# Performance work log

Hardware: AMD Instinct MI355X
Metric: run time of the kernel (lower is better)

The kernel has to match this reference:

```python
import jax, jax.numpy as jnp
import numpy as np

N = 100000   # nodes
E = 1600000  # edges
D = 128      # in_dim
H = 128      # hidden_dim
C = 40       # num_classes
EPS = 1e-5   # LayerNorm eps (torch default)


def setup_inputs() -> dict:
    key = jax.random.key(0)
    ks = jax.random.split(key, 16)
    x = jax.random.normal(ks[0], (N, D), dtype=jnp.float32)
    edge_index = jax.random.randint(ks[1], (2, E), 0, N, dtype=jnp.int64)
    s = 1.0 / np.sqrt(D)
    inp = {"x": x, "edge_index": edge_index}
    # 3 GCN layers: weight [in, H], bias [H]; LayerNorm gamma/beta [H]
    for i in range(3):
        inp[f"W{i}"] = jax.random.normal(ks[2 + i], (D if i == 0 else H, H), dtype=jnp.float32) * s
        inp[f"b{i}"] = jnp.zeros((H,), jnp.float32)
        inp[f"g{i}"] = jnp.ones((H,), jnp.float32)
        inp[f"be{i}"] = jnp.zeros((H,), jnp.float32)
    inp["Wc"] = jax.random.normal(ks[10], (H, C), dtype=jnp.float32) * (1.0 / np.sqrt(H))
    inp["bc"] = jnp.zeros((C,), jnp.float32)
    return inp


def _layer_norm(h, g, b):
    mu = jnp.mean(h, axis=-1, keepdims=True)
    var = jnp.var(h, axis=-1, keepdims=True)  # biased, matches torch
    return (h - mu) * jax.lax.rsqrt(var + EPS) * g + b


def _gcn_conv(x, W, b, src, dst, enorm, dinv2):
    # GCNConv: D^{-1/2}(A+I)D^{-1/2} X W + b (self-loops handled analytically)
    h = x @ W                                   # [N, H]
    agg = jax.ops.segment_sum(h[src] * enorm[:, None], dst, num_segments=N)
    return agg + h * dinv2[:, None] + b


def reference(x, edge_index, W0, b0, g0, be0, W1, b1, g1, be1, W2, b2, g2, be2, Wc, bc):
    src, dst = edge_index[0], edge_index[1]
    # degree with self-loops (GCNConv adds self-loops by default)
    deg = jnp.zeros((N,), x.dtype).at[dst].add(1.0) + 1.0
    dinv = jax.lax.rsqrt(deg)
    enorm = dinv[src] * dinv[dst]               # per-edge normalization
    dinv2 = dinv * dinv                         # self-loop normalization

    Ws, bs, gs, bes = (W0, W1, W2), (b0, b1, b2), (g0, g1, g2), (be0, be1, be2)
    for i in range(3):
        x_in = x
        x = _gcn_conv(x, Ws[i], bs[i], src, dst, enorm, dinv2)
        x = _layer_norm(x, gs[i], bes[i])
        x = jax.nn.elu(x)
        if i > 0:
            x = x + x_in
        # dropout: eval mode / p=0 -> identity
    return x @ Wc + bc
```

## Files before the change

kernel.cpp:

```cpp
#include <hip/hip_runtime.h>
#include <math.h>

#define N_NODES 100000
#define N_EDGES 1600000
#define DIM     128
#define NCLS    40
#define NBUCK   391
#define P1_CH   4096
#define CAP     8192

typedef _Float16 f16x8 __attribute__((ext_vector_type(8)));
typedef _Float16 f16x2 __attribute__((ext_vector_type(2)));
typedef float    f32x4 __attribute__((ext_vector_type(4)));

__device__ inline unsigned short f16bits(float f) {
    union { _Float16 h; unsigned short u; } cv;
    cv.h = (_Float16)f;
    return cv.u;
}
__device__ inline f16x2 as_h2(unsigned u) {
    union { unsigned u; f16x2 h; } cv;
    cv.u = u;
    return cv.h;
}
__device__ inline unsigned as_u(f16x2 h) {
    union { f16x2 h; unsigned u; } cv;
    cv.h = h;
    return cv.u;
}
__device__ inline unsigned pack_h2(float lo, float hi) {
    f16x2 h;
    h.x = (_Float16)lo;
    h.y = (_Float16)hi;
    return as_u(h);
}
__device__ inline int wave_incl_scan(int v, int lane) {
#pragma unroll
    for (int off = 1; off < 64; off <<= 1) {
        int x = __shfl_up(v, off, 64);
        if (lane >= off) v += x;
    }
    return v;
}

__global__ __launch_bounds__(256) void setup_p1(const float* __restrict__ W0,
                                                const float* __restrict__ W1,
                                                const float* __restrict__ W2,
                                                const float* __restrict__ Wc,
                                                const int* __restrict__ ei,
                                                unsigned short* __restrict__ Wsw0,
                                                unsigned short* __restrict__ Wsw1,
                                                unsigned short* __restrict__ Wsw2,
                                                unsigned short* __restrict__ Wcsw,
                                                int* __restrict__ bcnt,
                                                unsigned* __restrict__ tmp,
                                                unsigned short* __restrict__ H2) {
    const int blk = blockIdx.x;
    const int t   = threadIdx.x;

    if (blk < 192) {
        const float* W = (blk < 64) ? W0 : (blk < 128) ? W1 : W2;
        unsigned short* Wsw = (blk < 64) ? Wsw0 : (blk < 128) ? Wsw1 : Wsw2;
        int o = (blk & 63) * 256 + t;
        int f = o >> 9;
        int l = (o >> 3) & 63;
        int j = o & 7;
        int n = f >> 2;
        int s = f & 3;
        int k = s * 32 + (l >> 4) * 8 + j;
        int c = (l & 15) * 8 + n;
        Wsw[o] = f16bits(W[k * DIM + c]);
        return;
    }
    if (blk < 216) {
        int o = (blk - 192) * 256 + t;
        int f = o >> 9;
        int l = (o >> 3) & 63;
        int j = o & 7;
        int n = f >> 2;
        int s = f & 3;
        int k = s * 32 + (l >> 4) * 8 + j;
        int c = (l & 15) * 3 + n;
        Wcsw[o] = (c < NCLS) ? f16bits(Wc[k * NCLS + c]) : (unsigned short)0;
        return;
    }
    if (blk == 216) {
        uint4* p = (uint4*)(H2 + (size_t)N_NODES * DIM);
        uint4 zz = make_uint4(0u, 0u, 0u, 0u);
#pragma unroll
        for (int i = 0; i < 4; ++i) p[t + i * 256] = zz;
        return;
    }

    __shared__ int  hist[512];
    __shared__ int  lscan[512];
    __shared__ int  rank_[512];
    __shared__ int  gbase[512];
    __shared__ int  wtA[4];
    __shared__ int2 stage[P1_CH];

    const int lane = t & 63, wv = t >> 6;
    const int e0  = (blk - 217) * P1_CH;
    const int cnt = min(P1_CH, N_EDGES - e0);

    hist[t] = 0;
    hist[t + 256] = 0;
    __syncthreads();

    int2 ed[16];
#pragma unroll
    for (int i = 0; i < 16; ++i) {
        int idx = t + i * 256;
        if (idx < cnt) {
            ed[i] = make_int2(ei[e0 + idx], ei[N_EDGES + e0 + idx]);
            atomicAdd(&hist[ed[i].y >> 8], 1);
        }
    }
    __syncthreads();

    int h0 = hist[2 * t], h1 = hist[2 * t + 1];
    int pvA = h0 + h1;
    int iA = wave_incl_scan(pvA, lane);
    if (lane == 63) wtA[wv] = iA;
    __syncthreads();
    {
        int fA = 0;
        for (int i = 0; i < wv; ++i) fA += wtA[i];
        iA += fA;
    }
    int eA = iA - pvA;
    lscan[2 * t]     = eA;
    lscan[2 * t + 1] = eA + h0;
    rank_[2 * t]     = eA;
    rank_[2 * t + 1] = eA + h0;
    if (h0) {
        int off = atomicAdd(&bcnt[2 * t], h0);
        if (off > CAP - h0) off = CAP - h0;
        if (off < 0) off = 0;
        gbase[2 * t] = (2 * t) * CAP + off;
    }
    if (h1) {
        int off = atomicAdd(&bcnt[2 * t + 1], h1);
        if (off > CAP - h1) off = CAP - h1;
        if (off < 0) off = 0;
        gbase[2 * t + 1] = (2 * t + 1) * CAP + off;
    }
    __syncthreads();

#pragma unroll
    for (int i = 0; i < 16; ++i) {
        int idx = t + i * 256;
        if (idx < cnt) {
            int b = ed[i].y >> 8;
            int p = atomicAdd(&rank_[b], 1);
            stage[p] = ed[i];
        }
    }
    __syncthreads();

    for (int p = t; p < cnt; p += 256) {
        int2 v = stage[p];
        int b = v.y >> 8;
        int dstidx = gbase[b] + (p - lscan[b]);
        if (dstidx < (b + 1) * CAP)
            tmp[dstidx] = ((unsigned)v.x << 8) | ((unsigned)v.y & 255u);
    }
}

__global__ __launch_bounds__(256) void csr_p2_gemm(const unsigned* __restrict__ tmp,
                                                   const int* __restrict__ bcnt,
                                                   const float* __restrict__ X,
                                                   const unsigned short* __restrict__ Wsw,
                                                   int* __restrict__ rowptr,
                                                   float* __restrict__ dinv,
                                                   unsigned* __restrict__ rec,
                                                   unsigned short* __restrict__ H) {
    __shared__ unsigned short wlds[32 * 512];
    __shared__ int   cnt2[256];
    __shared__ int   cur[256];
    __shared__ float dv_s[256];
    __shared__ int   wt[4];
    __shared__ int   sbeg_s;
    const int t = threadIdx.x;
    const int lane = t & 63, wv = t >> 6;
    const int b = blockIdx.x;

    {
        const uint4* srcp = (const uint4*)Wsw;
        uint4*       dstp = (uint4*)wlds;
#pragma unroll
        for (int i = 0; i < 8; ++i) dstp[t + i * 256] = srcp[t + i * 256];
    }

    int v0 = min(bcnt[2 * t], CAP), v1 = min(bcnt[2 * t + 1], CAP);
    int pv = v0 + v1;
    int incl = wave_incl_scan(pv, lane);
    if (lane == 63) wt[wv] = incl;
    cnt2[t] = 0;
    __syncthreads();
    {
        int pf = 0;
        for (int i = 0; i < wv; ++i) pf += wt[i];
        incl += pf;
        int eB = incl - pv;
        if (2 * t == b)     sbeg_s = eB;
        if (2 * t + 1 == b) sbeg_s = eB + v0;
    }
    __syncthreads();

    const int m = min(bcnt[b], CAP);
    const unsigned* tb = tmp + (size_t)b * CAP;
    for (int idx = t; idx < m; idx += 256)
        atomicAdd(&cnt2[tb[idx] & 255u], 1);
    __syncthreads();

    int c = cnt2[t];
    int incl2 = wave_incl_scan(c, lane);
    if (lane == 63) wt[wv] = incl2;
    __syncthreads();
    {
        int pf = 0;
        for (int i = 0; i < wv; ++i) pf += wt[i];
        incl2 += pf;
    }
    int rb = sbeg_s + (incl2 - c);
    cur[t] = rb;
    float dv = rsqrtf((float)c + 1.0f);
    dv_s[t] = dv;
    const int node = (b << 8) + t;
    if (node < N_NODES) {
        rowptr[node] = rb;
        dinv[node]   = dv;
    }
    if (b == NBUCK - 1 && t == 0) rowptr[N_NODES] = N_EDGES;
    __syncthreads();

    for (int idx = t; idx < m; idx += 256) {
        unsigned u = tb[idx];
        int pos = atomicAdd(&cur[u & 255u], 1);
        if ((unsigned)pos < (unsigned)N_EDGES)
            rec[pos] = (u >> 8) << 8;
    }

    const int mq = lane & 15;
    const int q  = lane >> 4;
    const int rowbase = (b << 8) + wv * 64;

    for (int r4 = 0; r4 < 4; ++r4) {
        const int row0 = rowbase + r4 * 16;
        int r = row0 + mq;
        if (r >= N_NODES) r = N_NODES - 1;
        const float* xp = X + (size_t)r * DIM + q * 8;
        f16x8 af[4];
#pragma unroll
        for (int s = 0; s < 4; ++s) {
            float4 x0 = *(const float4*)(xp + s * 32);
            float4 x1 = *(const float4*)(xp + s * 32 + 4);
            f16x8 v;
            v[0] = (_Float16)x0.x; v[1] = (_Float16)x0.y;
            v[2] = (_Float16)x0.z; v[3] = (_Float16)x0.w;
            v[4] = (_Float16)x1.x; v[5] = (_Float16)x1.y;
            v[6] = (_Float16)x1.z; v[7] = (_Float16)x1.w;
            af[s] = v;
        }

        f32x4 acc[8];
        f32x4 z = {0.f, 0.f, 0.f, 0.f};
#pragma unroll
        for (int n = 0; n < 8; ++n) acc[n] = z;

        const unsigned short* wl = wlds + lane * 8;
#pragma unroll
        for (int s = 0; s < 4; ++s)
#pragma unroll
            for (int n = 0; n < 8; ++n) {
                f16x8 wf = *(const f16x8*)(wl + ((n * 4 + s) << 9));
                acc[n] = __builtin_amdgcn_mfma_f32_16x16x32_f16(af[s], wf, acc[n], 0, 0, 0);
            }

#pragma unroll
        for (int j = 0; j < 4; ++j) {
            int row = row0 + q * 4 + j;
            if (row < N_NODES) {
                float dvr = dv_s[row - (b << 8)];
                uint4 o;
                o.x = pack_h2(acc[0][j] * dvr, acc[1][j] * dvr);
                o.y = pack_h2(acc[2][j] * dvr, acc[3][j] * dvr);
                o.z = pack_h2(acc[4][j] * dvr, acc[5][j] * dvr);
                o.w = pack_h2(acc[6][j] * dvr, acc[7][j] * dvr);
                *(uint4*)(H + (size_t)row * DIM + mq * 8) = o;
            } else if (row < N_NODES + 32) {
                uint4 zz = make_uint4(0u, 0u, 0u, 0u);
                *(uint4*)(H + (size_t)row * DIM + mq * 8) = zz;
            }
        }
    }
}

__global__ __launch_bounds__(256) void agg_ln_gemm(const unsigned short* __restrict__ Hh,
                                                   const unsigned short* __restrict__ xin,
                                                   const float* __restrict__ dinv,
                                                   const float* __restrict__ bias,
                                                   const float* __restrict__ g,
                                                   const float* __restrict__ be,
                                                   const int* __restrict__ rowptr,
                                                   const unsigned* __restrict__ rec,
                                                   const unsigned short* __restrict__ Wsw,
                                                   unsigned short* __restrict__ Cout,
                                                   unsigned short* __restrict__ Hout) {
    __shared__ _Float16 hl[16][136];
    const int tid  = threadIdx.x;
    const int lane = tid & 63;
    const int l16  = tid & 15;
    const int gb   = lane & 48;
    const int grp  = tid >> 4;
    const int wave = tid >> 6;
    const int node0 = blockIdx.x * 16;
    const int node = node0 + grp;
    const int beg  = rowptr[node];
    const int end  = rowptr[node + 1];
    const char* Hb8 = (const char*)Hh;
    const unsigned laneoff = (unsigned)l16 * 16;
    const unsigned sentin  = (unsigned)N_NODES << 8;

    f16x2 accA[4], accB[4], accC[4], accD[4];
    f16x2 hz = {(_Float16)0.f, (_Float16)0.f};
#pragma unroll
    for (int k = 0; k < 4; ++k) { accA[k] = hz; accB[k] = hz; accC[k] = hz; accD[k] = hz; }

    for (int e0 = beg; e0 < end; e0 += 16) {
        int cnt = min(end - e0, 16);
        unsigned sv = (l16 < cnt) ? rec[e0 + l16] : sentin;
        int cntR = (cnt + 7) & ~7;
        for (int j = 0; j < cntR; j += 8) {
            unsigned o0 = (unsigned)__shfl((int)sv, gb + j + 0, 64) + laneoff;
            unsigned o1 = (unsigned)__shfl((int)sv, gb + j + 1, 64) + laneoff;
            unsigned o2 = (unsigned)__shfl((int)sv, gb + j + 2, 64) + laneoff;
            unsigned o3 = (unsigned)__shfl((int)sv, gb + j + 3, 64) + laneoff;
            unsigned o4 = (unsigned)__shfl((int)sv, gb + j + 4, 64) + laneoff;
            unsigned o5 = (unsigned)__shfl((int)sv, gb + j + 5, 64) + laneoff;
            unsigned o6 = (unsigned)__shfl((int)sv, gb + j + 6, 64) + laneoff;
            unsigned o7 = (unsigned)__shfl((int)sv, gb + j + 7, 64) + laneoff;
            uint4 u0 = *(const uint4*)(Hb8 + o0);
            uint4 u1 = *(const uint4*)(Hb8 + o1);
            uint4 u2 = *(const uint4*)(Hb8 + o2);
            uint4 u3 = *(const uint4*)(Hb8 + o3);
            uint4 u4 = *(const uint4*)(Hb8 + o4);
            uint4 u5 = *(const uint4*)(Hb8 + o5);
            uint4 u6 = *(const uint4*)(Hb8 + o6);
            uint4 u7 = *(const uint4*)(Hb8 + o7);
            accA[0] += as_h2(u0.x); accA[1] += as_h2(u0.y); accA[2] += as_h2(u0.z); accA[3] += as_h2(u0.w);
            accB[0] += as_h2(u1.x); accB[1] += as_h2(u1.y); accB[2] += as_h2(u1.z); accB[3] += as_h2(u1.w);
            accC[0] += as_h2(u2.x); accC[1] += as_h2(u2.y); accC[2] += as_h2(u2.z); accC[3] += as_h2(u2.w);
            accD[0] += as_h2(u3.x); accD[1] += as_h2(u3.y); accD[2] += as_h2(u3.z); accD[3] += as_h2(u3.w);
            accA[0] += as_h2(u4.x); accA[1] += as_h2(u4.y); accA[2] += as_h2(u4.z); accA[3] += as_h2(u4.w);
            accB[0] += as_h2(u5.x); accB[1] += as_h2(u5.y); accB[2] += as_h2(u5.z); accB[3] += as_h2(u5.w);
            accC[0] += as_h2(u6.x); accC[1] += as_h2(u6.y); accC[2] += as_h2(u6.z); accC[3] += as_h2(u6.w);
            accD[0] += as_h2(u7.x); accD[1] += as_h2(u7.y); accD[2] += as_h2(u7.z); accD[3] += as_h2(u7.w);
        }
    }

#pragma unroll
    for (int k = 0; k < 4; ++k) accA[k] = (accA[k] + accB[k]) + (accC[k] + accD[k]);

    const float dv = dinv[node];
    const unsigned nodeoff = ((unsigned)node << 8) + laneoff;
    uint4 hv = *(const uint4*)(Hb8 + nodeoff);
    const int c0 = l16 * 8;
    float4 bb0 = *(const float4*)(bias + c0);
    float4 bb1 = *(const float4*)(bias + c0 + 4);
    f16x2 h0 = as_h2(hv.x), h1 = as_h2(hv.y), h2 = as_h2(hv.z), h3 = as_h2(hv.w);

    float a[8];
    a[0] = ((float)accA[0].x + (float)h0.x) * dv + bb0.x;
    a[1] = ((float)accA[0].y + (float)h0.y) * dv + bb0.y;
    a[2] = ((float)accA[1].x + (float)h1.x) * dv + bb0.z;
    a[3] = ((float)accA[1].y + (float)h1.y) * dv + bb0.w;
    a[4] = ((float)accA[2].x + (float)h2.x) * dv + bb1.x;
    a[5] = ((float)accA[2].y + (float)h2.y) * dv + bb1.y;
    a[6] = ((float)accA[3].x + (float)h3.x) * dv + bb1.z;
    a[7] = ((float)accA[3].y + (float)h3.y) * dv + bb1.w;

    float s1 = 0.f, s2 = 0.f;
#pragma unroll
    for (int i = 0; i < 8; ++i) { s1 += a[i]; s2 += a[i] * a[i]; }
#pragma unroll
    for (int mk = 1; mk <= 8; mk <<= 1) {
        s1 += __shfl_xor(s1, mk, 64);
        s2 += __shfl_xor(s2, mk, 64);
    }
    float mean = s1 * (1.0f / 128.0f);
    float var  = s2 * (1.0f / 128.0f) - mean * mean;
    float rr   = rsqrtf(var + 1e-5f);

    float4 gg0 = *(const float4*)(g + c0);
    float4 gg1 = *(const float4*)(g + c0 + 4);
    float4 ee0 = *(const float4*)(be + c0);
    float4 ee1 = *(const float4*)(be + c0 + 4);

    float r[8];
    r[0] = (a[0] - mean) * rr * gg0.x + ee0.x;
    r[1] = (a[1] - mean) * rr * gg0.y + ee0.y;
    r[2] = (a[2] - mean) * rr * gg0.z + ee0.z;
    r[3] = (a[3] - mean) * rr * gg0.w + ee0.w;
    r[4] = (a[4] - mean) * rr * gg1.x + ee1.x;
    r[5] = (a[5] - mean) * rr * gg1.y + ee1.y;
    r[6] = (a[6] - mean) * rr * gg1.z + ee1.z;
    r[7] = (a[7] - mean) * rr * gg1.w + ee1.w;
#pragma unroll
    for (int i = 0; i < 8; ++i) r[i] = r[i] > 0.0f ? r[i] : expm1f(r[i]);

    if (xin) {
        uint4 xv = *(const uint4*)((const char*)xin + nodeoff);
        f16x2 x0 = as_h2(xv.x), x1 = as_h2(xv.y), x2 = as_h2(xv.z), x3 = as_h2(xv.w);
        r[0] += (float)x0.x; r[1] += (float)x0.y;
        r[2] += (float)x1.x; r[3] += (float)x1.y;
        r[4] += (float)x2.x; r[5] += (float)x2.y;
        r[6] += (float)x3.x; r[7] += (float)x3.y;
    }

    uint4 o;
    o.x = pack_h2(r[0], r[1]);
    o.y = pack_h2(r[2], r[3]);
    o.z = pack_h2(r[4], r[5]);
    o.w = pack_h2(r[6], r[7]);
    *(uint4*)((char*)Cout + nodeoff) = o;
    *(uint4*)&hl[grp][l16 * 8] = o;
    __syncthreads();

    {
        const int m = lane & 15;
        const int q = lane >> 4;

        f16x8 af[4];
#pragma unroll
        for (int s = 0; s < 4; ++s)
            af[s] = *(const f16x8*)&hl[m][q * 8 + s * 32];

        f32x4 acc2[2];
        f32x4 z = {0.f, 0.f, 0.f, 0.f};
        acc2[0] = z; acc2[1] = z;

#pragma unroll
        for (int s = 0; s < 4; ++s)
#pragma unroll
            for (int p = 0; p < 2; ++p) {
                f16x8 wfv = *(const f16x8*)(Wsw + (((2 * wave + p) * 4 + s) << 9) + lane * 8);
                acc2[p] = __builtin_amdgcn_mfma_f32_16x16x32_f16(af[s], wfv, acc2[p], 0, 0, 0);
            }

#pragma unroll
        for (int j = 0; j < 4; ++j) {
            int row = node0 + q * 4 + j;
            float dv2 = dinv[row];
            *(unsigned*)((char*)Hout + ((unsigned)row << 8) + ((unsigned)(m * 8 + 2 * wave) << 1)) =
                pack_h2(acc2[0][j] * dv2, acc2[1][j] * dv2);
        }
    }
}

__global__ __launch_bounds__(256) void agg_ln_cls(const unsigned short* __restrict__ Hh,
                                                  const unsigned short* __restrict__ xin,
                                                  const float* __restrict__ dinv,
                                                  const float* __restrict__ bias,
                                                  const float* __restrict__ g,
                                                  const float* __restrict__ be,
                                                  const int* __restrict__ rowptr,
                                                  const unsigned* __restrict__ rec,
                                                  const unsigned short* __restrict__ Wcsw,
                                                  const float* __restrict__ bc,
                                                  float* __restrict__ out) {
    __shared__ _Float16 hl[16][136];
    const int tid  = threadIdx.x;
    const int lane = tid & 63;
    const int l16  = tid & 15;
    const int gb   = lane & 48;
    const int grp  = tid >> 4;
    const int node0 = blockIdx.x * 16;
    const int node = node0 + grp;
    const int beg  = rowptr[node];
    const int end  = rowptr[node + 1];
    const char* Hb8 = (const char*)Hh;
    const unsigned laneoff = (unsigned)l16 * 16;
    const unsigned sentin  = (unsigned)N_NODES << 8;

    f16x2 accA[4], accB[4], accC[4], accD[4];
    f16x2 hz = {(_Float16)0.f, (_Float16)0.f};
#pragma unroll
    for (int k = 0; k < 4; ++k) { accA[k] = hz; accB[k] = hz; accC[k] = hz; accD[k] = hz; }

    for (int e0 = beg; e0 < end; e0 += 16) {
        int cnt = min(end - e0, 16);
        unsigned sv = (l16 < cnt) ? rec[e0 + l16] : sentin;
        int cntR = (cnt + 7) & ~7;
        for (int j = 0; j < cntR; j += 8) {
            unsigned o0 = (unsigned)__shfl((int)sv, gb + j + 0, 64) + laneoff;
            unsigned o1 = (unsigned)__shfl((int)sv, gb + j + 1, 64) + laneoff;
            unsigned o2 = (unsigned)__shfl((int)sv, gb + j + 2, 64) + laneoff;
            unsigned o3 = (unsigned)__shfl((int)sv, gb + j + 3, 64) + laneoff;
            unsigned o4 = (unsigned)__shfl((int)sv, gb + j + 4, 64) + laneoff;
            unsigned o5 = (unsigned)__shfl((int)sv, gb + j + 5, 64) + laneoff;
            unsigned o6 = (unsigned)__shfl((int)sv, gb + j + 6, 64) + laneoff;
            unsigned o7 = (unsigned)__shfl((int)sv, gb + j + 7, 64) + laneoff;
            uint4 u0 = *(const uint4*)(Hb8 + o0);
            uint4 u1 = *(const uint4*)(Hb8 + o1);
            uint4 u2 = *(const uint4*)(Hb8 + o2);
            uint4 u3 = *(const uint4*)(Hb8 + o3);
            uint4 u4 = *(const uint4*)(Hb8 + o4);
            uint4 u5 = *(const uint4*)(Hb8 + o5);
            uint4 u6 = *(const uint4*)(Hb8 + o6);
            uint4 u7 = *(const uint4*)(Hb8 + o7);
            accA[0] += as_h2(u0.x); accA[1] += as_h2(u0.y); accA[2] += as_h2(u0.z); accA[3] += as_h2(u0.w);
            accB[0] += as_h2(u1.x); accB[1] += as_h2(u1.y); accB[2] += as_h2(u1.z); accB[3] += as_h2(u1.w);
            accC[0] += as_h2(u2.x); accC[1] += as_h2(u2.y); accC[2] += as_h2(u2.z); accC[3] += as_h2(u2.w);
            accD[0] += as_h2(u3.x); accD[1] += as_h2(u3.y); accD[2] += as_h2(u3.z); accD[3] += as_h2(u3.w);
            accA[0] += as_h2(u4.x); accA[1] += as_h2(u4.y); accA[2] += as_h2(u4.z); accA[3] += as_h2(u4.w);
            accB[0] += as_h2(u5.x); accB[1] += as_h2(u5.y); accB[2] += as_h2(u5.z); accB[3] += as_h2(u5.w);
            accC[0] += as_h2(u6.x); accC[1] += as_h2(u6.y); accC[2] += as_h2(u6.z); accC[3] += as_h2(u6.w);
            accD[0] += as_h2(u7.x); accD[1] += as_h2(u7.y); accD[2] += as_h2(u7.z); accD[3] += as_h2(u7.w);
        }
    }

#pragma unroll
    for (int k = 0; k < 4; ++k) accA[k] = (accA[k] + accB[k]) + (accC[k] + accD[k]);

    const float dv = dinv[node];
    const unsigned nodeoff = ((unsigned)node << 8) + laneoff;
    uint4 hv = *(const uint4*)(Hb8 + nodeoff);
    const int c0 = l16 * 8;
    float4 bb0 = *(const float4*)(bias + c0);
    float4 bb1 = *(const float4*)(bias + c0 + 4);
    f16x2 h0 = as_h2(hv.x), h1 = as_h2(hv.y), h2 = as_h2(hv.z), h3 = as_h2(hv.w);

    float a[8];
    a[0] = ((float)accA[0].x + (float)h0.x) * dv + bb0.x;
    a[1] = ((float)accA[0].y + (float)h0.y) * dv + bb0.y;
    a[2] = ((float)accA[1].x + (float)h1.x) * dv + bb0.z;
    a[3] = ((float)accA[1].y + (float)h1.y) * dv + bb0.w;
    a[4] = ((float)accA[2].x + (float)h2.x) * dv + bb1.x;
    a[5] = ((float)accA[2].y + (float)h2.y) * dv + bb1.y;
    a[6] = ((float)accA[3].x + (float)h3.x) * dv + bb1.z;
    a[7] = ((float)accA[3].y + (float)h3.y) * dv + bb1.w;

    float s1 = 0.f, s2 = 0.f;
#pragma unroll
    for (int i = 0; i < 8; ++i) { s1 += a[i]; s2 += a[i] * a[i]; }
#pragma unroll
    for (int mk = 1; mk <= 8; mk <<= 1) {
        s1 += __shfl_xor(s1, mk, 64);
        s2 += __shfl_xor(s2, mk, 64);
    }
    float mean = s1 * (1.0f / 128.0f);
    float var  = s2 * (1.0f / 128.0f) - mean * mean;
    float rr   = rsqrtf(var + 1e-5f);

    float4 gg0 = *(const float4*)(g + c0);
    float4 gg1 = *(const float4*)(g + c0 + 4);
    float4 ee0 = *(const float4*)(be + c0);
    float4 ee1 = *(const float4*)(be + c0 + 4);

    float r[8];
    r[0] = (a[0] - mean) * rr * gg0.x + ee0.x;
    r[1] = (a[1] - mean) * rr * gg0.y + ee0.y;
    r[2] = (a[2] - mean) * rr * gg0.z + ee0.z;
    r[3] = (a[3] - mean) * rr * gg0.w + ee0.w;
    r[4] = (a[4] - mean) * rr * gg1.x + ee1.x;
    r[5] = (a[5] - mean) * rr * gg1.y + ee1.y;
    r[6] = (a[6] - mean) * rr * gg1.z + ee1.z;
    r[7] = (a[7] - mean) * rr * gg1.w + ee1.w;
#pragma unroll
    for (int i = 0; i < 8; ++i) r[i] = r[i] > 0.0f ? r[i] : expm1f(r[i]);

    if (xin) {
        uint4 xv = *(const uint4*)((const char*)xin + nodeoff);
        f16x2 x0 = as_h2(xv.x), x1 = as_h2(xv.y), x2 = as_h2(xv.z), x3 = as_h2(xv.w);
        r[0] += (float)x0.x; r[1] += (float)x0.y;
        r[2] += (float)x1.x; r[3] += (float)x1.y;
        r[4] += (float)x2.x; r[5] += (float)x2.y;
        r[6] += (float)x3.x; r[7] += (float)x3.y;
    }

    uint4 o;
    o.x = pack_h2(r[0], r[1]);
    o.y = pack_h2(r[2], r[3]);
    o.z = pack_h2(r[4], r[5]);
    o.w = pack_h2(r[6], r[7]);
    *(uint4*)&hl[grp][l16 * 8] = o;
    __syncthreads();

    if (tid < 64) {
        const int m = lane & 15;
        const int q = lane >> 4;

        f16x8 wf[12];
#pragma unroll
        for (int f = 0; f < 12; ++f)
            wf[f] = *(const f16x8*)(Wcsw + (f << 9) + lane * 8);

        f16x8 af[4];
#pragma unroll
        for (int s = 0; s < 4; ++s)
            af[s] = *(const f16x8*)&hl[m][q * 8 + s * 32];

        f32x4 acc[3];
        f32x4 z = {0.f, 0.f, 0.f, 0.f};
#pragma unroll
        for (int n = 0; n < 3; ++n) acc[n] = z;

#pragma unroll
        for (int s = 0; s < 4; ++s)
#pragma unroll
            for (int n = 0; n < 3; ++n)
                acc[n] = __builtin_amdgcn_mfma_f32_16x16x32_f16(af[s], wf[n * 4 + s], acc[n], 0, 0, 0);

#pragma unroll
        for (int j = 0; j < 4; ++j) {
            int row = node0 + q * 4 + j;
#pragma unroll
            for (int n = 0; n < 3; ++n) {
                int c = 3 * m + n;
                if (c < NCLS)
                    out[(size_t)row * NCLS + c] = acc[n][j] + bc[c];
            }
        }
    }
}

extern "C" void kernel_launch(void* const* d_in, const int* in_sizes, int n_in,
                              void* d_out, int out_size, void* d_ws, size_t ws_size,
                              hipStream_t stream) {
    const float* x  = (const float*)d_in[0];
    const int*   ei = (const int*)d_in[1];
    const float* W[3]  = {(const float*)d_in[2], (const float*)d_in[6], (const float*)d_in[10]};
    const float* b[3]  = {(const float*)d_in[3], (const float*)d_in[7], (const float*)d_in[11]};
    const float* g[3]  = {(const float*)d_in[4], (const float*)d_in[8], (const float*)d_in[12]};
    const float* be[3] = {(const float*)d_in[5], (const float*)d_in[9], (const float*)d_in[13]};
    const float* Wc = (const float*)d_in[14];
    const float* bc = (const float*)d_in[15];
    float* out = (float*)d_out;

    char* ws = (char*)d_ws;
    const size_t NP = 400128;
    float* dinv   = (float*)(ws);
    int*   rowptr = (int*)  (ws + NP);
    int*   bcnt   = (int*)  (ws + 2 * NP);
    unsigned* rec = (unsigned*)(ws + 2 * NP + 4096);
    unsigned short* H1 = (unsigned short*)(ws + 2 * NP + 4096 + (size_t)N_EDGES * 8);
    unsigned short* H2 = H1 + (size_t)(N_NODES + 64) * DIM;
    unsigned short* Ch = H2 + (size_t)(N_NODES + 64) * DIM;
    unsigned short* Wsw0 = Ch + (size_t)N_NODES * DIM;
    unsigned short* Wsw1 = Wsw0 + DIM * DIM;
    unsigned short* Wsw2 = Wsw1 + DIM * DIM;
    unsigned short* Wcsw = Wsw2 + DIM * DIM;
    unsigned* tmp = (unsigned*)Ch;

    hipMemsetAsync(bcnt, 0, 2048, stream);

    setup_p1<<<217 + NBUCK, 256, 0, stream>>>(W[0], W[1], W[2], Wc, ei,
                                              Wsw0, Wsw1, Wsw2, Wcsw, bcnt, tmp, H2);

    csr_p2_gemm<<<NBUCK, 256, 0, stream>>>(tmp, bcnt, x, Wsw0, rowptr, dinv, rec, H1);

    const int agg_grid = N_NODES / 16;

    agg_ln_gemm<<<agg_grid, 256, 0, stream>>>(H1, nullptr, dinv, b[0], g[0], be[0],
                                              rowptr, rec, Wsw1, Ch, H2);

    agg_ln_gemm<<<agg_grid, 256, 0, stream>>>(H2, Ch, dinv, b[1], g[1], be[1],
                                              rowptr, rec, Wsw2, Ch, H1);

    agg_ln_cls<<<agg_grid, 256, 0, stream>>>(H1, Ch, dinv, b[2], g[2], be[2],
                                             rowptr, rec, Wcsw, bc, out);
}
```

Before: 365.7 us.

## Replace global atomic bucket offsets with per-chunk count matrix and fixed slots

Edge binning no longer reserves space in each destination bucket with global atomics. Each edge chunk writes its per-bucket histogram into a bucket-by-chunk count matrix and places its edges in a fixed 32-entry slot per (bucket, chunk). A new small reduction kernel sums the matrix rows into bucket totals, and the CSR pass walks the padded slots, skipping empty entries. This removes the memset and the global atomics and makes the layout deterministic. In exchange it adds a kernel launch, more padded reads in the CSR pass, and silently drops edges if any chunk puts more than 32 edges into one bucket.

```diff
diff --git a/kernel.cpp b/kernel.cpp
--- a/kernel.cpp
+++ b/kernel.cpp
@@ -7,7 +7,7 @@
 #define NCLS    40
 #define NBUCK   391
 #define P1_CH   4096
-#define CAP     8192
+#define CAPB    32
 
 typedef _Float16 f16x8 __attribute__((ext_vector_type(8)));
 typedef _Float16 f16x2 __attribute__((ext_vector_type(2)));
@@ -52,7 +52,7 @@
                                                 unsigned short* __restrict__ Wsw1,
                                                 unsigned short* __restrict__ Wsw2,
                                                 unsigned short* __restrict__ Wcsw,
-                                                int* __restrict__ bcnt,
+                                                int* __restrict__ cntmat,
                                                 unsigned* __restrict__ tmp,
                                                 unsigned short* __restrict__ H2) {
     const int blk = blockIdx.x;
@@ -95,12 +95,12 @@
     __shared__ int  hist[512];
     __shared__ int  lscan[512];
     __shared__ int  rank_[512];
-    __shared__ int  gbase[512];
     __shared__ int  wtA[4];
     __shared__ int2 stage[P1_CH];
 
     const int lane = t & 63, wv = t >> 6;
-    const int e0  = (blk - 217) * P1_CH;
+    const int k   = blk - 217;
+    const int e0  = k * P1_CH;
     const int cnt = min(P1_CH, N_EDGES - e0);
 
     hist[t] = 0;
@@ -133,18 +133,8 @@
     lscan[2 * t + 1] = eA + h0;
     rank_[2 * t]     = eA;
     rank_[2 * t + 1] = eA + h0;
-    if (h0) {
-        int off = atomicAdd(&bcnt[2 * t], h0);
-        if (off > CAP - h0) off = CAP - h0;
-        if (off < 0) off = 0;
-        gbase[2 * t] = (2 * t) * CAP + off;
-    }
-    if (h1) {
-        int off = atomicAdd(&bcnt[2 * t + 1], h1);
-        if (off > CAP - h1) off = CAP - h1;
-        if (off < 0) off = 0;
-        gbase[2 * t + 1] = (2 * t + 1) * CAP + off;
-    }
+    if (2 * t < NBUCK)     cntmat[(size_t)(2 * t) * NBUCK + k]     = h0;
+    if (2 * t + 1 < NBUCK) cntmat[(size_t)(2 * t + 1) * NBUCK + k] = h1;
     __syncthreads();
 
 #pragma unroll
@@ -161,13 +151,28 @@
     for (int p = t; p < cnt; p += 256) {
         int2 v = stage[p];
         int b = v.y >> 8;
-        int dstidx = gbase[b] + (p - lscan[b]);
-        if (dstidx < (b + 1) * CAP)
-            tmp[dstidx] = ((unsigned)v.x << 8) | ((unsigned)v.y & 255u);
-    }
+        int r = p - lscan[b];
+        if (r < CAPB)
+            tmp[((size_t)b * NBUCK + k) * CAPB + r] = ((unsigned)v.x << 8) | ((unsigned)v.y & 255u);
+    }
+}
+
+__global__ __launch_bounds__(256) void bsum(const int* __restrict__ cntmat,
+                                            int* __restrict__ bcnt) {
+    const int gw   = (blockIdx.x * 256 + threadIdx.x) >> 6;
+    const int lane = threadIdx.x & 63;
+    int s = 0;
+    if (gw < NBUCK) {
+        const int* row = cntmat + (size_t)gw * NBUCK;
+        for (int i = lane; i < NBUCK; i += 64) s += row[i];
+#pragma unroll
+        for (int m = 1; m < 64; m <<= 1) s += __shfl_xor(s, m, 64);
+    }
+    if (gw < 512 && lane == 0) bcnt[gw] = s;
 }
 
 __global__ __launch_bounds__(256) void csr_p2_gemm(const unsigned* __restrict__ tmp,
+                                                   const int* __restrict__ cntmat,
                                                    const int* __restrict__ bcnt,
                                                    const float* __restrict__ X,
                                                    const unsigned short* __restrict__ Wsw,
@@ -176,6 +181,7 @@
                                                    unsigned* __restrict__ rec,
                                                    unsigned short* __restrict__ H) {
     __shared__ unsigned short wlds[32 * 512];
+    __shared__ int   cnts[512];
     __shared__ int   cnt2[256];
     __shared__ int   cur[256];
     __shared__ float dv_s[256];
@@ -192,7 +198,10 @@
         for (int i = 0; i < 8; ++i) dstp[t + i * 256] = srcp[t + i * 256];
     }
 
-    int v0 = min(bcnt[2 * t], CAP), v1 = min(bcnt[2 * t + 1], CAP);
+    cnts[t]       = (t < NBUCK)       ? cntmat[(size_t)b * NBUCK + t]       : 0;
+    cnts[t + 256] = (t + 256 < NBUCK) ? cntmat[(size_t)b * NBUCK + t + 256] : 0;
+
+    int v0 = bcnt[2 * t], v1 = bcnt[2 * t + 1];
     int pv = v0 + v1;
     int incl = wave_incl_scan(pv, lane);
     if (lane == 63) wt[wv] = incl;
@@ -208,10 +217,11 @@
     }
     __syncthreads();
 
-    const int m = min(bcnt[b], CAP);
-    const unsigned* tb = tmp + (size_t)b * CAP;
-    for (int idx = t; idx < m; idx += 256)
-        atomicAdd(&cnt2[tb[idx] & 255u], 1);
+    const unsigned* tb = tmp + (size_t)b * (NBUCK * CAPB);
+    for (int s = t; s < NBUCK * CAPB; s += 256) {
+        if ((s & (CAPB - 1)) < cnts[s >> 5])
+            atomicAdd(&cnt2[tb[s] & 255u], 1);
+    }
     __syncthreads();
 
     int c = cnt2[t];
@@ -235,11 +245,13 @@
     if (b == NBUCK - 1 && t == 0) rowptr[N_NODES] = N_EDGES;
     __syncthreads();
 
-    for (int idx = t; idx < m; idx += 256) {
-        unsigned u = tb[idx];
-        int pos = atomicAdd(&cur[u & 255u], 1);
-        if ((unsigned)pos < (unsigned)N_EDGES)
-            rec[pos] = (u >> 8) << 8;
+    for (int s = t; s < NBUCK * CAPB; s += 256) {
+        if ((s & (CAPB - 1)) < cnts[s >> 5]) {
+            unsigned u = tb[s];
+            int pos = atomicAdd(&cur[u & 255u], 1);
+            if ((unsigned)pos < (unsigned)N_EDGES)
+                rec[pos] = (u >> 8) << 8;
+        }
     }
 
     const int mq = lane & 15;
@@ -652,14 +664,15 @@
     unsigned short* Wsw1 = Wsw0 + DIM * DIM;
     unsigned short* Wsw2 = Wsw1 + DIM * DIM;
     unsigned short* Wcsw = Wsw2 + DIM * DIM;
+    int* cntmat = (int*)(Wcsw + 12 * 512);
     unsigned* tmp = (unsigned*)Ch;
 
-    hipMemsetAsync(bcnt, 0, 2048, stream);
-
     setup_p1<<<217 + NBUCK, 256, 0, stream>>>(W[0], W[1], W[2], Wc, ei,
-                                              Wsw0, Wsw1, Wsw2, Wcsw, bcnt, tmp, H2);
-
-    csr_p2_gemm<<<NBUCK, 256, 0, stream>>>(tmp, bcnt, x, Wsw0, rowptr, dinv, rec, H1);
+                                              Wsw0, Wsw1, Wsw2, Wcsw, cntmat, tmp, H2);
+
+    bsum<<<128, 256, 0, stream>>>(cntmat, bcnt);
+
+    csr_p2_gemm<<<NBUCK, 256, 0, stream>>>(tmp, cntmat, bcnt, x, Wsw0, rowptr, dinv, rec, H1);
 
     const int agg_grid = N_NODES / 16;
 
```

Result: slower. 373.3 us (+2.1%).
